# Kernel optimization log

Hardware: AMD Instinct MI355X
Metric: run time of the kernel (lower is better)

The kernel has to match this reference:

```python
import jax, jax.numpy as jnp
import numpy as np

B, NB, DIM = 4096, 64, 256
CNT_R = 500
CNT_E = CNT_R * 2  # padding relation id == CNT_E maps to the masked row
N_WR = CNT_R * 2 + 1
N_ZQ = CNT_R * 2


def setup_inputs() -> dict:
    key = jax.random.key(0)
    ks = jax.random.split(key, 10)
    batch_nei_rid = jax.random.randint(ks[0], (B, NB), 0, N_WR, dtype=jnp.int64 if jax.config.read('jax_enable_x64') else jnp.int32)
    batch_nei_e_emb = jax.random.normal(ks[1], (B, NB, DIM), dtype=jnp.float32)
    batch_nei_rw = jax.random.uniform(ks[2], (B, NB), dtype=jnp.float32)
    batch_q_rid = jax.random.randint(ks[3], (B,), 0, N_ZQ, dtype=jnp.int32)
    # xavier-normal-ish params
    def xav(k, shape):
        fan_in, fan_out = shape[-1], shape[-2] if len(shape) > 1 else shape[-1]
        std = (2.0 / (fan_in + fan_out)) ** 0.5
        return (jax.random.normal(k, shape) * std).astype(jnp.float32)
    w_r_weight = xav(ks[4], (N_WR, DIM))
    zq_weight = xav(ks[5], (N_ZQ, DIM))
    attn_W_w = xav(ks[6], (2 * DIM, 2 * DIM))   # [out, in], torch Linear layout
    attn_W_b = jnp.zeros((2 * DIM,), jnp.float32)
    u_a_w = xav(ks[7], (1, 2 * DIM))
    u_a_b = jnp.zeros((1,), jnp.float32)
    return {
        'batch_nei_rid': batch_nei_rid,
        'batch_nei_e_emb': batch_nei_e_emb,
        'batch_nei_rw': batch_nei_rw,
        'batch_q_rid': batch_q_rid,
        'w_r_weight': w_r_weight,
        'zq_weight': zq_weight,
        'attn_W_w': attn_W_w,
        'attn_W_b': attn_W_b,
        'u_a_w': u_a_w,
        'u_a_b': u_a_b,
    }


def reference(batch_nei_rid, batch_nei_e_emb, batch_nei_rw, batch_q_rid,
              w_r_weight, zq_weight, attn_W_w, attn_W_b, u_a_w, u_a_b):
    # relation hyperplane gather + TransH-style projection
    w_r = w_r_weight[batch_nei_rid]                                   # [B,NB,D]
    nrm = jnp.maximum(jnp.linalg.norm(w_r, axis=-1, keepdims=True), 1e-12)
    wn = w_r / nrm                                                    # f.normalize(p=2)
    e_tr = batch_nei_e_emb - jnp.sum(batch_nei_e_emb * wn, axis=-1, keepdims=True) * wn
    # mask_emb: 1 for real rows, 0 for padding row (index CNT_E)
    mask = (batch_nei_rid < CNT_E).astype(e_tr.dtype)[..., None]
    e_tr = e_tr * mask
    # nn attention: concat(z_q, e_Tr) -> Linear -> tanh -> Linear(1)
    z_q = zq_weight[batch_q_rid][:, None, :]                          # [B,1,D]
    cat = jnp.concatenate([jnp.broadcast_to(z_q, e_tr.shape), e_tr], axis=-1)  # [B,NB,2D]
    h = jnp.tanh(jnp.einsum('bni,oi->bno', cat, attn_W_w) + attn_W_b)
    _alpha = jnp.einsum('bni,oi->bno', h, u_a_w)[..., 0] + u_a_b[0]   # [B,NB]
    # mask_weight: 1e19 at padding row, subtracted before softmax
    _alpha = _alpha - jnp.where(batch_nei_rid == CNT_E, jnp.asarray(1e19, _alpha.dtype), jnp.asarray(0.0, _alpha.dtype))
    alpha = jax.nn.softmax(_alpha, axis=-1)
    attn = alpha + batch_nei_rw                                       # use_logic_attention
    return jnp.sum(attn[..., None] * e_tr, axis=-2)                   # [B,D]
```

## Files before the change

### kernel.cpp

```cpp
#include <hip/hip_runtime.h>
#include <math.h>

#define NB    64
#define DIM   256
#define TWOD  512
#define CNTE  1000
#define E2S   264
#define NQ    1000

typedef __attribute__((ext_vector_type(8))) short short8;
typedef __attribute__((ext_vector_type(4))) float f32x4;

union U16x8 { uint4 u; short8 s; };

__device__ __forceinline__ unsigned short f2bf(float x) {
    unsigned int u = __float_as_uint(x);
    u += 0x7fffu + ((u >> 16) & 1u);
    return (unsigned short)(u >> 16);
}
__device__ __forceinline__ float bf2f(unsigned short h) {
    return __uint_as_float(((unsigned int)h) << 16);
}

__global__ __launch_bounds__(256) void zpre_kernel(
    const float* __restrict__ zq_w, const float* __restrict__ attn_W,
    const float* __restrict__ attn_b, float* __restrict__ zpre)
{
    __shared__ float zq[8][DIM];
    const int t  = threadIdx.x;
    const int q0 = blockIdx.x * 8;
    #pragma unroll
    for (int r = 0; r < 8; ++r) zq[r][t] = zq_w[(size_t)(q0 + r) * DIM + t];
    __syncthreads();
    #pragma unroll
    for (int half = 0; half < 2; ++half) {
        const int o = t + half * 256;
        const float4* wrow = (const float4*)(attn_W + (size_t)o * TWOD);
        float acc[8];
        #pragma unroll
        for (int r = 0; r < 8; ++r) acc[r] = 0.f;
        #pragma unroll 4
        for (int kk = 0; kk < 64; ++kk) {
            float4 w = wrow[kk];
            #pragma unroll
            for (int r = 0; r < 8; ++r)
                acc[r] += w.x * zq[r][kk * 4 + 0] + w.y * zq[r][kk * 4 + 1]
                        + w.z * zq[r][kk * 4 + 2] + w.w * zq[r][kk * 4 + 3];
        }
        const float bo = attn_b[o];
        #pragma unroll
        for (int r = 0; r < 8; ++r)
            zpre[(size_t)(q0 + r) * TWOD + o] = acc[r] + bo;
    }
}

__global__ __launch_bounds__(256) void pack_w_kernel(
    const float* __restrict__ attn_W, unsigned short* __restrict__ wbf)
{
    int f = blockIdx.x * 256 + threadIdx.x;
    int j    = f & 7;
    int lane = (f >> 3) & 63;
    int kt   = (f >> 9) & 7;
    int ot   = f >> 12;
    int o  = ot * 16 + (lane & 15);
    int ke = kt * 32 + (lane >> 4) * 8 + j;
    wbf[f] = f2bf(attn_W[(size_t)o * TWOD + 256 + ke]);
}

__global__ __launch_bounds__(256, 2) void encoder_attn_kernel(
    const int*   __restrict__ nei_rid,
    const float* __restrict__ nei_e,
    const float* __restrict__ nei_rw,
    const int*   __restrict__ q_rid,
    const float* __restrict__ w_r,
    const float* __restrict__ zq_w,
    const float* __restrict__ attn_W,
    const float* __restrict__ attn_b,
    const float* __restrict__ u_a_w,
    const float* __restrict__ zpre,
    const unsigned short* __restrict__ wbf,
    float*       __restrict__ out,
    int has_zpre)
{
    __shared__ __align__(16) unsigned short e2[NB * E2S];
    __shared__ float2 zu[TWOD];
    __shared__ __align__(16) float red_a[256];
    __shared__ float  pen[NB];
    __shared__ float  attn_lds[NB];

    const int b = blockIdx.x;
    const int t = threadIdx.x;
    const int qr = q_rid[b];

    if (has_zpre) {
        zu[t]       = make_float2(zpre[(size_t)qr * TWOD + t],       u_a_w[t]);
        zu[t + 256] = make_float2(zpre[(size_t)qr * TWOD + t + 256], u_a_w[t + 256]);
    } else {
        red_a[t] = zq_w[(size_t)qr * DIM + t];
        __syncthreads();
        float a0 = 0.f, a1 = 0.f;
        const float4* w0 = (const float4*)(attn_W + (size_t)t * TWOD);
        const float4* w1 = (const float4*)(attn_W + (size_t)(t + 256) * TWOD);
        const float4* zz = (const float4*)red_a;
        #pragma unroll 8
        for (int kk = 0; kk < 64; ++kk) {
            float4 z = zz[kk], u0 = w0[kk], u1 = w1[kk];
            a0 += u0.x * z.x + u0.y * z.y + u0.z * z.z + u0.w * z.w;
            a1 += u1.x * z.x + u1.y * z.y + u1.z * z.z + u1.w * z.w;
        }
        zu[t]       = make_float2(a0 + attn_b[t],       u_a_w[t]);
        zu[t + 256] = make_float2(a1 + attn_b[t + 256], u_a_w[t + 256]);
        __syncthreads();
    }

    {
        const int q = t & 7;
        #pragma unroll
        for (int half = 0; half < 2; ++half) {
            const int n = (t >> 3) + half * 32;
            const int rid = nei_rid[b * NB + n];
            const float4* e4 = (const float4*)(nei_e + ((size_t)(b * NB + n)) * DIM) + q * 8;
            const float4* w4 = (const float4*)(w_r + (size_t)rid * DIM) + q * 8;
            float4 ev[8], wv[8];
            float sew = 0.f, sww = 0.f;
            #pragma unroll
            for (int j = 0; j < 8; ++j) {
                ev[j] = e4[j]; wv[j] = w4[j];
                sew += ev[j].x * wv[j].x + ev[j].y * wv[j].y + ev[j].z * wv[j].z + ev[j].w * wv[j].w;
                sww += wv[j].x * wv[j].x + wv[j].y * wv[j].y + wv[j].z * wv[j].z + wv[j].w * wv[j].w;
            }
            sew += __shfl_xor(sew, 1); sew += __shfl_xor(sew, 2); sew += __shfl_xor(sew, 4);
            sww += __shfl_xor(sww, 1); sww += __shfl_xor(sww, 2); sww += __shfl_xor(sww, 4);
            float nc   = fmaxf(sqrtf(sww), 1e-12f);
            float coef = sew / (nc * nc);
            float maskf = (rid < CNTE) ? 1.f : 0.f;
            if (q == 0) pen[n] = (rid == CNTE) ? 1e19f : 0.f;
            unsigned short* e2row = e2 + n * E2S + q * 32;
            #pragma unroll
            for (int jj = 0; jj < 4; ++jj) {
                float4 e0 = ev[jj * 2],     w0 = wv[jj * 2];
                float4 e1 = ev[jj * 2 + 1], w1 = wv[jj * 2 + 1];
                uint4 pk;
                pk.x = (unsigned int)f2bf((e0.x - coef * w0.x) * maskf)
                     | ((unsigned int)f2bf((e0.y - coef * w0.y) * maskf) << 16);
                pk.y = (unsigned int)f2bf((e0.z - coef * w0.z) * maskf)
                     | ((unsigned int)f2bf((e0.w - coef * w0.w) * maskf) << 16);
                pk.z = (unsigned int)f2bf((e1.x - coef * w1.x) * maskf)
                     | ((unsigned int)f2bf((e1.y - coef * w1.y) * maskf) << 16);
                pk.w = (unsigned int)f2bf((e1.z - coef * w1.z) * maskf)
                     | ((unsigned int)f2bf((e1.w - coef * w1.w) * maskf) << 16);
                *(uint4*)(e2row + jj * 8) = pk;
            }
        }
    }
    __syncthreads();

    const int wv_id = t >> 6;
    const int lane  = t & 63;
    const int l15 = lane & 15, lq = lane >> 4;

    f32x4 acc[8][4];
    #pragma unroll
    for (int oo = 0; oo < 8; ++oo) {
        const float zx = zu[(wv_id * 8 + oo) * 16 + l15].x;
        #pragma unroll
        for (int mt = 0; mt < 4; ++mt) acc[oo][mt] = (f32x4){zx, zx, zx, zx};
    }

    #pragma unroll
    for (int kt = 0; kt < 8; ++kt) {
        short8 afr[4];
        #pragma unroll
        for (int mt = 0; mt < 4; ++mt) {
            U16x8 u; u.u = *(const uint4*)(e2 + (mt * 16 + l15) * E2S + kt * 32 + lq * 8);
            afr[mt] = u.s;
        }
        #pragma unroll
        for (int oo = 0; oo < 8; ++oo) {
            U16x8 u;
            u.u = ((const uint4*)wbf)[(size_t)((wv_id * 8 + oo) * 8 + kt) * 64 + lane];
            #pragma unroll
            for (int mt = 0; mt < 4; ++mt)
                acc[oo][mt] = __builtin_amdgcn_mfma_f32_16x16x32_bf16(
                                  afr[mt], u.s, acc[oo][mt], 0, 0, 0);
        }
    }

    f32x4 lpv[4];
    #pragma unroll
    for (int mt = 0; mt < 4; ++mt) lpv[mt] = (f32x4){0.f, 0.f, 0.f, 0.f};
    #pragma unroll
    for (int oo = 0; oo < 8; ++oo) {
        const float uy2 = -2.0f * zu[(wv_id * 8 + oo) * 16 + l15].y;
        #pragma unroll
        for (int mt = 0; mt < 4; ++mt)
            #pragma unroll
            for (int r = 0; r < 4; ++r) {
                float x = acc[oo][mt][r];
                float e = __expf(x + x);
                lpv[mt][r] += uy2 * __builtin_amdgcn_rcpf(e + 1.0f);
            }
    }

    #pragma unroll
    for (int mt = 0; mt < 4; ++mt)
        #pragma unroll
        for (int r = 0; r < 4; ++r) {
            float v = lpv[mt][r];
            v += __shfl_xor(v, 1); v += __shfl_xor(v, 2);
            v += __shfl_xor(v, 4); v += __shfl_xor(v, 8);
            if (l15 == 0) red_a[wv_id * 64 + mt * 16 + lq * 4 + r] = v;
        }
    __syncthreads();

    if (t < NB) {
        float lgt = red_a[t] + red_a[64 + t] + red_a[128 + t] + red_a[192 + t]
                  - pen[t];
        float m = lgt;
        #pragma unroll
        for (int off = 32; off > 0; off >>= 1) m = fmaxf(m, __shfl_xor(m, off));
        float ex = __expf(lgt - m);
        float s = ex;
        #pragma unroll
        for (int off = 32; off > 0; off >>= 1) s += __shfl_xor(s, off);
        attn_lds[t] = ex / s + nei_rw[b * NB + t];
    }
    __syncthreads();

    float oacc = 0.f;
    #pragma unroll 8
    for (int nn = 0; nn < NB; ++nn)
        oacc += attn_lds[nn] * bf2f(e2[nn * E2S + t]);
    out[(size_t)b * DIM + t] = oacc;
}

extern "C" void kernel_launch(void* const* d_in, const int* in_sizes, int n_in,
                              void* d_out, int out_size, void* d_ws, size_t ws_size,
                              hipStream_t stream) {
    const int*   nei_rid = (const int*)  d_in[0];
    const float* nei_e   = (const float*)d_in[1];
    const float* nei_rw  = (const float*)d_in[2];
    const int*   q_rid   = (const int*)  d_in[3];
    const float* w_r     = (const float*)d_in[4];
    const float* zq_w    = (const float*)d_in[5];
    const float* attn_W  = (const float*)d_in[6];
    const float* attn_b  = (const float*)d_in[7];
    const float* u_a_w   = (const float*)d_in[8];

    float* out = (float*)d_out;
    const int B = in_sizes[3];

    const size_t ZPRE_BYTES = (size_t)NQ * TWOD * 4;
    const size_t WBF_BYTES  = (size_t)512 * 256 * 2;
    const int has_zpre = (ws_size >= ZPRE_BYTES + WBF_BYTES) ? 1 : 0;

    float*          zpre = (float*)d_ws;
    unsigned short* wbf  = has_zpre
        ? (unsigned short*)((char*)d_ws + ZPRE_BYTES)
        : (unsigned short*)d_ws;

    if (has_zpre)
        hipLaunchKernelGGL(zpre_kernel, dim3(NQ / 8), dim3(256), 0, stream,
                           zq_w, attn_W, attn_b, zpre);
    hipLaunchKernelGGL(pack_w_kernel, dim3(512), dim3(256), 0, stream, attn_W, wbf);
    hipLaunchKernelGGL(encoder_attn_kernel, dim3(B), dim3(256), 0, stream,
                       nei_rid, nei_e, nei_rw, q_rid, w_r, zq_w, attn_W, attn_b,
                       u_a_w, zpre, wbf, out, has_zpre);
}
```

Before: 586.1 us.

## Restructure attention MFMA loop with preloaded A fragments and double-buffered weights

The main kernel now loads all A fragments of the projected neighbour embeddings from LDS into registers once. It then walks the output tiles one at a time, double-buffering the bf16 weight fragments from global memory so the next tile's loads overlap the current tile's MFMAs and tanh epilogue. This cuts the live accumulator set from 32 to 4 vectors. The projection stage now gives each thread a quarter row (4 threads per neighbour), and zpre_kernel is split across a second grid dimension with 128-thread blocks to raise parallelism. The trade-off is higher register use from the 32 held A fragments and the two weight buffers, which may hurt occupancy.

```diff
diff --git a/kernel.cpp b/kernel.cpp
--- a/kernel.cpp
+++ b/kernel.cpp
@@ -22,36 +22,36 @@
     return __uint_as_float(((unsigned int)h) << 16);
 }
 
-__global__ __launch_bounds__(256) void zpre_kernel(
+__global__ __launch_bounds__(128) void zpre_kernel(
     const float* __restrict__ zq_w, const float* __restrict__ attn_W,
     const float* __restrict__ attn_b, float* __restrict__ zpre)
 {
     __shared__ float zq[8][DIM];
     const int t  = threadIdx.x;
     const int q0 = blockIdx.x * 8;
-    #pragma unroll
-    for (int r = 0; r < 8; ++r) zq[r][t] = zq_w[(size_t)(q0 + r) * DIM + t];
-    __syncthreads();
-    #pragma unroll
-    for (int half = 0; half < 2; ++half) {
-        const int o = t + half * 256;
-        const float4* wrow = (const float4*)(attn_W + (size_t)o * TWOD);
-        float acc[8];
-        #pragma unroll
-        for (int r = 0; r < 8; ++r) acc[r] = 0.f;
-        #pragma unroll 4
-        for (int kk = 0; kk < 64; ++kk) {
-            float4 w = wrow[kk];
-            #pragma unroll
-            for (int r = 0; r < 8; ++r)
-                acc[r] += w.x * zq[r][kk * 4 + 0] + w.y * zq[r][kk * 4 + 1]
-                        + w.z * zq[r][kk * 4 + 2] + w.w * zq[r][kk * 4 + 3];
-        }
-        const float bo = attn_b[o];
+    const int o  = blockIdx.y * 128 + t;
+    #pragma unroll
+    for (int r = 0; r < 8; ++r) {
+        zq[r][t]       = zq_w[(size_t)(q0 + r) * DIM + t];
+        zq[r][t + 128] = zq_w[(size_t)(q0 + r) * DIM + t + 128];
+    }
+    __syncthreads();
+    const float4* wrow = (const float4*)(attn_W + (size_t)o * TWOD);
+    float acc[8];
+    #pragma unroll
+    for (int r = 0; r < 8; ++r) acc[r] = 0.f;
+    #pragma unroll 8
+    for (int kk = 0; kk < 64; ++kk) {
+        float4 w = wrow[kk];
         #pragma unroll
         for (int r = 0; r < 8; ++r)
-            zpre[(size_t)(q0 + r) * TWOD + o] = acc[r] + bo;
-    }
+            acc[r] += w.x * zq[r][kk * 4 + 0] + w.y * zq[r][kk * 4 + 1]
+                    + w.z * zq[r][kk * 4 + 2] + w.w * zq[r][kk * 4 + 3];
+    }
+    const float bo = attn_b[o];
+    #pragma unroll
+    for (int r = 0; r < 8; ++r)
+        zpre[(size_t)(q0 + r) * TWOD + o] = acc[r] + bo;
 }
 
 __global__ __launch_bounds__(256) void pack_w_kernel(
@@ -114,43 +114,39 @@
     }
 
     {
-        const int q = t & 7;
-        #pragma unroll
-        for (int half = 0; half < 2; ++half) {
-            const int n = (t >> 3) + half * 32;
-            const int rid = nei_rid[b * NB + n];
-            const float4* e4 = (const float4*)(nei_e + ((size_t)(b * NB + n)) * DIM) + q * 8;
-            const float4* w4 = (const float4*)(w_r + (size_t)rid * DIM) + q * 8;
-            float4 ev[8], wv[8];
-            float sew = 0.f, sww = 0.f;
-            #pragma unroll
-            for (int j = 0; j < 8; ++j) {
-                ev[j] = e4[j]; wv[j] = w4[j];
-                sew += ev[j].x * wv[j].x + ev[j].y * wv[j].y + ev[j].z * wv[j].z + ev[j].w * wv[j].w;
-                sww += wv[j].x * wv[j].x + wv[j].y * wv[j].y + wv[j].z * wv[j].z + wv[j].w * wv[j].w;
-            }
-            sew += __shfl_xor(sew, 1); sew += __shfl_xor(sew, 2); sew += __shfl_xor(sew, 4);
-            sww += __shfl_xor(sww, 1); sww += __shfl_xor(sww, 2); sww += __shfl_xor(sww, 4);
-            float nc   = fmaxf(sqrtf(sww), 1e-12f);
-            float coef = sew / (nc * nc);
-            float maskf = (rid < CNTE) ? 1.f : 0.f;
-            if (q == 0) pen[n] = (rid == CNTE) ? 1e19f : 0.f;
-            unsigned short* e2row = e2 + n * E2S + q * 32;
-            #pragma unroll
-            for (int jj = 0; jj < 4; ++jj) {
-                float4 e0 = ev[jj * 2],     w0 = wv[jj * 2];
-                float4 e1 = ev[jj * 2 + 1], w1 = wv[jj * 2 + 1];
-                uint4 pk;
-                pk.x = (unsigned int)f2bf((e0.x - coef * w0.x) * maskf)
-                     | ((unsigned int)f2bf((e0.y - coef * w0.y) * maskf) << 16);
-                pk.y = (unsigned int)f2bf((e0.z - coef * w0.z) * maskf)
-                     | ((unsigned int)f2bf((e0.w - coef * w0.w) * maskf) << 16);
-                pk.z = (unsigned int)f2bf((e1.x - coef * w1.x) * maskf)
-                     | ((unsigned int)f2bf((e1.y - coef * w1.y) * maskf) << 16);
-                pk.w = (unsigned int)f2bf((e1.z - coef * w1.z) * maskf)
-                     | ((unsigned int)f2bf((e1.w - coef * w1.w) * maskf) << 16);
-                *(uint4*)(e2row + jj * 8) = pk;
-            }
+        const int n = t >> 2, q = t & 3;
+        const int rid = nei_rid[b * NB + n];
+        const float4* e4 = (const float4*)(nei_e + ((size_t)(b * NB + n)) * DIM) + q * 16;
+        const float4* w4 = (const float4*)(w_r + (size_t)rid * DIM) + q * 16;
+        float4 ev[16], wv[16];
+        float sew = 0.f, sww = 0.f;
+        #pragma unroll
+        for (int j = 0; j < 16; ++j) {
+            ev[j] = e4[j]; wv[j] = w4[j];
+            sew += ev[j].x * wv[j].x + ev[j].y * wv[j].y + ev[j].z * wv[j].z + ev[j].w * wv[j].w;
+            sww += wv[j].x * wv[j].x + wv[j].y * wv[j].y + wv[j].z * wv[j].z + wv[j].w * wv[j].w;
+        }
+        sew += __shfl_xor(sew, 1); sew += __shfl_xor(sew, 2);
+        sww += __shfl_xor(sww, 1); sww += __shfl_xor(sww, 2);
+        float nc   = fmaxf(sqrtf(sww), 1e-12f);
+        float coef = sew / (nc * nc);
+        float maskf = (rid < CNTE) ? 1.f : 0.f;
+        if (q == 0) pen[n] = (rid == CNTE) ? 1e19f : 0.f;
+        unsigned short* e2row = e2 + n * E2S + q * 64;
+        #pragma unroll
+        for (int jj = 0; jj < 8; ++jj) {
+            float4 e0 = ev[jj * 2],     w0 = wv[jj * 2];
+            float4 e1 = ev[jj * 2 + 1], w1 = wv[jj * 2 + 1];
+            uint4 pk;
+            pk.x = (unsigned int)f2bf((e0.x - coef * w0.x) * maskf)
+                 | ((unsigned int)f2bf((e0.y - coef * w0.y) * maskf) << 16);
+            pk.y = (unsigned int)f2bf((e0.z - coef * w0.z) * maskf)
+                 | ((unsigned int)f2bf((e0.w - coef * w0.w) * maskf) << 16);
+            pk.z = (unsigned int)f2bf((e1.x - coef * w1.x) * maskf)
+                 | ((unsigned int)f2bf((e1.y - coef * w1.y) * maskf) << 16);
+            pk.w = (unsigned int)f2bf((e1.z - coef * w1.z) * maskf)
+                 | ((unsigned int)f2bf((e1.w - coef * w1.w) * maskf) << 16);
+            *(uint4*)(e2row + jj * 8) = pk;
         }
     }
     __syncthreads();
@@ -159,48 +155,60 @@
     const int lane  = t & 63;
     const int l15 = lane & 15, lq = lane >> 4;
 
-    f32x4 acc[8][4];
-    #pragma unroll
-    for (int oo = 0; oo < 8; ++oo) {
-        const float zx = zu[(wv_id * 8 + oo) * 16 + l15].x;
-        #pragma unroll
-        for (int mt = 0; mt < 4; ++mt) acc[oo][mt] = (f32x4){zx, zx, zx, zx};
-    }
-
-    #pragma unroll
-    for (int kt = 0; kt < 8; ++kt) {
-        short8 afr[4];
-        #pragma unroll
-        for (int mt = 0; mt < 4; ++mt) {
+    short8 afrag[4][8];
+    #pragma unroll
+    for (int mt = 0; mt < 4; ++mt)
+        #pragma unroll
+        for (int kt = 0; kt < 8; ++kt) {
             U16x8 u; u.u = *(const uint4*)(e2 + (mt * 16 + l15) * E2S + kt * 32 + lq * 8);
-            afr[mt] = u.s;
-        }
-        #pragma unroll
-        for (int oo = 0; oo < 8; ++oo) {
-            U16x8 u;
-            u.u = ((const uint4*)wbf)[(size_t)((wv_id * 8 + oo) * 8 + kt) * 64 + lane];
-            #pragma unroll
-            for (int mt = 0; mt < 4; ++mt)
-                acc[oo][mt] = __builtin_amdgcn_mfma_f32_16x16x32_bf16(
-                                  afr[mt], u.s, acc[oo][mt], 0, 0, 0);
-        }
-    }
+            afrag[mt][kt] = u.s;
+        }
 
     f32x4 lpv[4];
     #pragma unroll
     for (int mt = 0; mt < 4; ++mt) lpv[mt] = (f32x4){0.f, 0.f, 0.f, 0.f};
-    #pragma unroll
-    for (int oo = 0; oo < 8; ++oo) {
-        const float uy2 = -2.0f * zu[(wv_id * 8 + oo) * 16 + l15].y;
-        #pragma unroll
-        for (int mt = 0; mt < 4; ++mt)
-            #pragma unroll
-            for (int r = 0; r < 4; ++r) {
-                float x = acc[oo][mt][r];
-                float e = __expf(x + x);
-                lpv[mt][r] += uy2 * __builtin_amdgcn_rcpf(e + 1.0f);
-            }
-    }
+
+    const uint4* wbase = (const uint4*)wbf + (size_t)(wv_id * 8) * 512 + lane;
+
+    uint4 bufA[8], bufB[8];
+    #pragma unroll
+    for (int kt = 0; kt < 8; ++kt) bufA[kt] = wbase[kt * 64];
+
+#define PROC_OT(OT, CUR, NXT, NOT)                                              \
+    {                                                                           \
+        _Pragma("unroll")                                                       \
+        for (int kt = 0; kt < 8; ++kt) NXT[kt] = wbase[(NOT) * 512 + kt * 64];  \
+        const int otg = wv_id * 8 + (OT);                                       \
+        const float2 zub = zu[otg * 16 + l15];                                  \
+        f32x4 acc[4];                                                           \
+        _Pragma("unroll")                                                       \
+        for (int mt = 0; mt < 4; ++mt)                                          \
+            acc[mt] = (f32x4){zub.x, zub.x, zub.x, zub.x};                      \
+        _Pragma("unroll")                                                       \
+        for (int kt = 0; kt < 8; ++kt) {                                        \
+            U16x8 u; u.u = CUR[kt];                                             \
+            _Pragma("unroll")                                                   \
+            for (int mt = 0; mt < 4; ++mt)                                      \
+                acc[mt] = __builtin_amdgcn_mfma_f32_16x16x32_bf16(              \
+                              afrag[mt][kt], u.s, acc[mt], 0, 0, 0);            \
+        }                                                                       \
+        const float uy2 = -2.0f * zub.y;                                        \
+        _Pragma("unroll")                                                       \
+        for (int mt = 0; mt < 4; ++mt)                                          \
+            _Pragma("unroll")                                                   \
+            for (int r = 0; r < 4; ++r) {                                       \
+                float x = acc[mt][r];                                           \
+                float e = __expf(x + x);                                        \
+                lpv[mt][r] += uy2 * __builtin_amdgcn_rcpf(e + 1.0f);            \
+            }                                                                   \
+    }
+
+    #pragma unroll 1
+    for (int i = 0; i < 4; ++i) {
+        PROC_OT(2 * i,     bufA, bufB, 2 * i + 1)
+        PROC_OT(2 * i + 1, bufB, bufA, (2 * i + 2) & 7)
+    }
+#undef PROC_OT
 
     #pragma unroll
     for (int mt = 0; mt < 4; ++mt)
@@ -260,7 +268,7 @@
         : (unsigned short*)d_ws;
 
     if (has_zpre)
-        hipLaunchKernelGGL(zpre_kernel, dim3(NQ / 8), dim3(256), 0, stream,
+        hipLaunchKernelGGL(zpre_kernel, dim3(NQ / 8, 4), dim3(128), 0, stream,
                            zq_w, attn_W, attn_b, zpre);
     hipLaunchKernelGGL(pack_w_kernel, dim3(512), dim3(256), 0, stream, attn_W, wbf);
     hipLaunchKernelGGL(encoder_attn_kernel, dim3(B), dim3(256), 0, stream,
```

Measured after the change: 543.1 us. 1.08x faster.

## Restructure MFMA loop to cut registers and raise occupancy; split zpre grid

Applied to the files above, without the earlier changes.

The main kernel's launch bound goes from 2 to 4 blocks per SU. The MFMA stage is rewritten to process the 64 neighbour rows in two halves and the output tiles one at a time, each with its own tanh epilogue, so only two accumulators are live instead of 32. The neighbour-projection loop is no longer unrolled, which also lowers register pressure. The zpre precompute kernel is split across a 2D grid of 128-thread blocks for more parallelism. The trade-off is that A fragments are reloaded from LDS per half and there is less instruction-level parallelism between MFMAs.

```diff
diff --git a/kernel.cpp b/kernel.cpp
--- a/kernel.cpp
+++ b/kernel.cpp
@@ -22,36 +22,36 @@
     return __uint_as_float(((unsigned int)h) << 16);
 }
 
-__global__ __launch_bounds__(256) void zpre_kernel(
+__global__ __launch_bounds__(128) void zpre_kernel(
     const float* __restrict__ zq_w, const float* __restrict__ attn_W,
     const float* __restrict__ attn_b, float* __restrict__ zpre)
 {
     __shared__ float zq[8][DIM];
     const int t  = threadIdx.x;
     const int q0 = blockIdx.x * 8;
+    const int o  = blockIdx.y * 128 + t;
     #pragma unroll
-    for (int r = 0; r < 8; ++r) zq[r][t] = zq_w[(size_t)(q0 + r) * DIM + t];
-    __syncthreads();
+    for (int r = 0; r < 8; ++r) {
+        zq[r][t]       = zq_w[(size_t)(q0 + r) * DIM + t];
+        zq[r][t + 128] = zq_w[(size_t)(q0 + r) * DIM + t + 128];
+    }
+    __syncthreads();
+    const float4* wrow = (const float4*)(attn_W + (size_t)o * TWOD);
+    float acc[8];
     #pragma unroll
-    for (int half = 0; half < 2; ++half) {
-        const int o = t + half * 256;
-        const float4* wrow = (const float4*)(attn_W + (size_t)o * TWOD);
-        float acc[8];
-        #pragma unroll
-        for (int r = 0; r < 8; ++r) acc[r] = 0.f;
-        #pragma unroll 4
-        for (int kk = 0; kk < 64; ++kk) {
-            float4 w = wrow[kk];
-            #pragma unroll
-            for (int r = 0; r < 8; ++r)
-                acc[r] += w.x * zq[r][kk * 4 + 0] + w.y * zq[r][kk * 4 + 1]
-                        + w.z * zq[r][kk * 4 + 2] + w.w * zq[r][kk * 4 + 3];
-        }
-        const float bo = attn_b[o];
+    for (int r = 0; r < 8; ++r) acc[r] = 0.f;
+    #pragma unroll 8
+    for (int kk = 0; kk < 64; ++kk) {
+        float4 w = wrow[kk];
         #pragma unroll
         for (int r = 0; r < 8; ++r)
-            zpre[(size_t)(q0 + r) * TWOD + o] = acc[r] + bo;
-    }
+            acc[r] += w.x * zq[r][kk * 4 + 0] + w.y * zq[r][kk * 4 + 1]
+                    + w.z * zq[r][kk * 4 + 2] + w.w * zq[r][kk * 4 + 3];
+    }
+    const float bo = attn_b[o];
+    #pragma unroll
+    for (int r = 0; r < 8; ++r)
+        zpre[(size_t)(q0 + r) * TWOD + o] = acc[r] + bo;
 }
 
 __global__ __launch_bounds__(256) void pack_w_kernel(
@@ -67,7 +67,7 @@
     wbf[f] = f2bf(attn_W[(size_t)o * TWOD + 256 + ke]);
 }
 
-__global__ __launch_bounds__(256, 2) void encoder_attn_kernel(
+__global__ __launch_bounds__(256, 4) void encoder_attn_kernel(
     const int*   __restrict__ nei_rid,
     const float* __restrict__ nei_e,
     const float* __restrict__ nei_rw,
@@ -115,7 +115,7 @@
 
     {
         const int q = t & 7;
-        #pragma unroll
+        #pragma unroll 1
         for (int half = 0; half < 2; ++half) {
             const int n = (t >> 3) + half * 32;
             const int rid = nei_rid[b * NB + n];
@@ -158,59 +158,65 @@
     const int wv_id = t >> 6;
     const int lane  = t & 63;
     const int l15 = lane & 15, lq = lane >> 4;
-
-    f32x4 acc[8][4];
-    #pragma unroll
-    for (int oo = 0; oo < 8; ++oo) {
-        const float zx = zu[(wv_id * 8 + oo) * 16 + l15].x;
-        #pragma unroll
-        for (int mt = 0; mt < 4; ++mt) acc[oo][mt] = (f32x4){zx, zx, zx, zx};
-    }
-
-    #pragma unroll
-    for (int kt = 0; kt < 8; ++kt) {
-        short8 afr[4];
-        #pragma unroll
-        for (int mt = 0; mt < 4; ++mt) {
-            U16x8 u; u.u = *(const uint4*)(e2 + (mt * 16 + l15) * E2S + kt * 32 + lq * 8);
-            afr[mt] = u.s;
+    const uint4* wbase = (const uint4*)wbf + (size_t)(wv_id * 8) * 512 + lane;
+
+    #pragma unroll 1
+    for (int mh = 0; mh < 2; ++mh) {
+        short8 af[2][8];
+        #pragma unroll
+        for (int mt = 0; mt < 2; ++mt)
+            #pragma unroll
+            for (int kt = 0; kt < 8; ++kt) {
+                U16x8 u;
+                u.u = *(const uint4*)(e2 + ((mh * 2 + mt) * 16 + l15) * E2S + kt * 32 + lq * 8);
+                af[mt][kt] = u.s;
+            }
+
+        f32x4 lpv[2];
+        lpv[0] = (f32x4){0.f, 0.f, 0.f, 0.f};
+        lpv[1] = (f32x4){0.f, 0.f, 0.f, 0.f};
+
+        #pragma unroll 1
+        for (int ot = 0; ot < 8; ++ot) {
+            uint4 bb[8];
+            #pragma unroll
+            for (int kt = 0; kt < 8; ++kt) bb[kt] = wbase[ot * 512 + kt * 64];
+
+            const int otg = wv_id * 8 + ot;
+            const float2 zub = zu[otg * 16 + l15];
+            f32x4 acc[2];
+            acc[0] = (f32x4){zub.x, zub.x, zub.x, zub.x};
+            acc[1] = acc[0];
+
+            #pragma unroll
+            for (int kt = 0; kt < 8; ++kt) {
+                U16x8 u; u.u = bb[kt];
+                acc[0] = __builtin_amdgcn_mfma_f32_16x16x32_bf16(af[0][kt], u.s, acc[0], 0, 0, 0);
+                acc[1] = __builtin_amdgcn_mfma_f32_16x16x32_bf16(af[1][kt], u.s, acc[1], 0, 0, 0);
+            }
+
+            const float uy2 = -2.0f * zub.y;
+            #pragma unroll
+            for (int mt = 0; mt < 2; ++mt)
+                #pragma unroll
+                for (int r = 0; r < 4; ++r) {
+                    float x = acc[mt][r];
+                    float e = __expf(x + x);
+                    lpv[mt][r] += uy2 * __builtin_amdgcn_rcpf(e + 1.0f);
+                }
         }
-        #pragma unroll
-        for (int oo = 0; oo < 8; ++oo) {
-            U16x8 u;
-            u.u = ((const uint4*)wbf)[(size_t)((wv_id * 8 + oo) * 8 + kt) * 64 + lane];
-            #pragma unroll
-            for (int mt = 0; mt < 4; ++mt)
-                acc[oo][mt] = __builtin_amdgcn_mfma_f32_16x16x32_bf16(
-                                  afr[mt], u.s, acc[oo][mt], 0, 0, 0);
-        }
-    }
-
-    f32x4 lpv[4];
-    #pragma unroll
-    for (int mt = 0; mt < 4; ++mt) lpv[mt] = (f32x4){0.f, 0.f, 0.f, 0.f};
-    #pragma unroll
-    for (int oo = 0; oo < 8; ++oo) {
-        const float uy2 = -2.0f * zu[(wv_id * 8 + oo) * 16 + l15].y;
-        #pragma unroll
-        for (int mt = 0; mt < 4; ++mt)
+
+        #pragma unroll
+        for (int mt = 0; mt < 2; ++mt)
             #pragma unroll
             for (int r = 0; r < 4; ++r) {
-                float x = acc[oo][mt][r];
-                float e = __expf(x + x);
-                lpv[mt][r] += uy2 * __builtin_amdgcn_rcpf(e + 1.0f);
-            }
-    }
-
-    #pragma unroll
-    for (int mt = 0; mt < 4; ++mt)
-        #pragma unroll
-        for (int r = 0; r < 4; ++r) {
-            float v = lpv[mt][r];
-            v += __shfl_xor(v, 1); v += __shfl_xor(v, 2);
-            v += __shfl_xor(v, 4); v += __shfl_xor(v, 8);
-            if (l15 == 0) red_a[wv_id * 64 + mt * 16 + lq * 4 + r] = v;
-        }
+                float v = lpv[mt][r];
+                v += __shfl_xor(v, 1); v += __shfl_xor(v, 2);
+                v += __shfl_xor(v, 4); v += __shfl_xor(v, 8);
+                if (l15 == 0)
+                    red_a[wv_id * 64 + (mh * 2 + mt) * 16 + lq * 4 + r] = v;
+            }
+    }
     __syncthreads();
 
     if (t < NB) {
@@ -260,7 +266,7 @@
         : (unsigned short*)d_ws;
 
     if (has_zpre)
-        hipLaunchKernelGGL(zpre_kernel, dim3(NQ / 8), dim3(256), 0, stream,
+        hipLaunchKernelGGL(zpre_kernel, dim3(NQ / 8, 4), dim3(128), 0, stream,
                            zq_w, attn_W, attn_b, zpre);
     hipLaunchKernelGGL(pack_w_kernel, dim3(512), dim3(256), 0, stream, attn_W, wbf);
     hipLaunchKernelGGL(encoder_attn_kernel, dim3(B), dim3(256), 0, stream,
```

Result: faster. 502.4 us (-14.3%).
